# Kernel tuning notes

Measured on AMD Instinct MI355X. Metric: run time of the kernel, lower is better.

The kernel has to match this reference:

```python
import jax, jax.numpy as jnp
import numpy as np

N_NODES = 50000
N_EDGES = 800000
HID = 128
EDGE_IN = 2 * HID + 4 + 20  # 2*hidden + edge_feat_dim + num_r_gaussian = 280


def setup_inputs() -> dict:
    key = jax.random.key(0)
    ks = jax.random.split(key, 16)
    s = lambda fan_in: 1.0 / np.sqrt(fan_in)
    inp = {
        "h": jax.random.normal(ks[0], (N_NODES, HID), dtype=jnp.float32),
        "edge_index": jax.random.randint(ks[1], (2, N_EDGES), 0, N_NODES, dtype=jnp.int64) if jax.config.jax_enable_x64 else jax.random.randint(ks[1], (2, N_EDGES), 0, N_NODES, dtype=jnp.int32),
        "edge_attr": jax.random.normal(ks[2], (N_EDGES, 24), dtype=jnp.float32),
        # edge_mlp: Linear(280->128) relu Linear(128->128) relu (act_last=True)
        "We1": jax.random.uniform(ks[3], (EDGE_IN, HID), jnp.float32, -s(EDGE_IN), s(EDGE_IN)),
        "be1": jnp.zeros((HID,), jnp.float32),
        "We2": jax.random.uniform(ks[4], (HID, HID), jnp.float32, -s(HID), s(HID)),
        "be2": jnp.zeros((HID,), jnp.float32),
        # edge_inf: Linear(128->1) + sigmoid
        "Wg": jax.random.uniform(ks[5], (HID, 1), jnp.float32, -s(HID), s(HID)),
        "bg": jnp.zeros((1,), jnp.float32),
        # node_mlp: Linear(256->128) relu Linear(128->128)
        "Wn1": jax.random.uniform(ks[6], (2 * HID, HID), jnp.float32, -s(2 * HID), s(2 * HID)),
        "bn1": jnp.zeros((HID,), jnp.float32),
        "Wn2": jax.random.uniform(ks[7], (HID, HID), jnp.float32, -s(HID), s(HID)),
        "bn2": jnp.zeros((HID,), jnp.float32),
    }
    return inp


def reference(h, edge_index, edge_attr, We1, be1, We2, be2, Wg, bg, Wn1, bn1, Wn2, bn2):
    dst, src = edge_index[0], edge_index[1]
    hi, hj = h[dst], h[src]                       # [E, HID] each
    x = jnp.concatenate([edge_attr, hi, hj], -1)  # [E, 280]
    mij = jax.nn.relu(jax.nn.relu(x @ We1 + be1) @ We2 + be2)  # [E, HID]
    eij = jax.nn.sigmoid(mij @ Wg + bg)           # [E, 1]
    mi = jax.ops.segment_sum(mij * eij, dst, num_segments=h.shape[0])  # [N, HID]
    y = jnp.concatenate([mi, h], -1)              # [N, 2*HID]
    out = jax.nn.relu(y @ Wn1 + bn1) @ Wn2 + bn2  # [N, HID]
    return out
```

## Files before the change

kernel.cpp:

```cpp
#include <hip/hip_runtime.h>

#define N_NODES 50000
#define N_EDGES 800000
#define HID 128

typedef _Float16 f16;
typedef _Float16 half8 __attribute__((ext_vector_type(8)));
typedef _Float16 half4 __attribute__((ext_vector_type(4)));
typedef _Float16 half2v __attribute__((ext_vector_type(2)));
typedef float f32x4 __attribute__((ext_vector_type(4)));
typedef float f32x2 __attribute__((ext_vector_type(2)));

#define OFF_MI     0UL
#define OFF_H16C   25600000UL
#define OFF_WC     38400000UL
#define OFF_CNT    38604800UL
#define OFF_CUR    38805504UL
#define OFF_E4     39006208UL
#define CSR_TOTAL  51806208UL

#define OFF_FMI  0UL
#define OFF_FH16 25600000UL
#define OFF_FW   38400000UL

#define WB1 0
#define WB2 36864
#define WN1 53248
#define WN2 86016

#define TS 136
#define YS 264
#define AS 40

#define EB 32
#define NB 32

__global__ __launch_bounds__(256) void pack_weights(
    const float* __restrict__ We1, const float* __restrict__ We2,
    const float* __restrict__ Wn1, const float* __restrict__ Wn2,
    f16* __restrict__ W, int* __restrict__ cnt, float* __restrict__ mi) {
  int i = blockIdx.x * 256 + threadIdx.x;
  if (cnt && i < 50176) cnt[i] = 0;
  if (mi) {
    f32x4 z = {0.f, 0.f, 0.f, 0.f};
    for (int j = i; j < N_NODES * HID / 4; j += 102400)
      ((f32x4*)mi)[j] = z;
  }
  if (i < 36864) {
    int j = i & 7, n = (i >> 3) & 127, qk = i >> 10;
    int k = qk * 8 + j;
    float v = 0.f;
    if (k < 256) v = We1[(24 + k) * 128 + n];
    else if (k < 280) v = We1[(k - 256) * 128 + n];
    W[WB1 + i] = (f16)v;
  } else if (i < 53248) {
    int l = i - 36864;
    int j = l & 7, n = (l >> 3) & 127, qk = l >> 10;
    W[WB2 + l] = (f16)We2[(qk * 8 + j) * 128 + n];
  } else if (i < 86016) {
    int l = i - 53248;
    int j = l & 7, n = (l >> 3) & 127, qk = l >> 10;
    W[WN1 + l] = (f16)Wn1[(qk * 8 + j) * 128 + n];
  } else if (i < 102400) {
    int l = i - 86016;
    int j = l & 7, n = (l >> 3) & 127, qk = l >> 10;
    W[WN2 + l] = (f16)Wn2[(qk * 8 + j) * 128 + n];
  }
}

__global__ __launch_bounds__(256) void scan_kernel(const int* __restrict__ cnt,
                                                   int* __restrict__ cur) {
  __shared__ int red[4];
  __shared__ int wsum[4];
  int t = threadIdx.x, b = blockIdx.x;
  int lane = t & 63, w = t >> 6;
  int s0 = 0;
  for (int i = t * 4; i < b * 1024; i += 1024) {
    int4 v = *(const int4*)(cnt + i);
    s0 += v.x + v.y + v.z + v.w;
  }
  #pragma unroll
  for (int off = 32; off; off >>= 1) s0 += __shfl_down(s0, off, 64);
  if (lane == 0) red[w] = s0;
  __syncthreads();
  int base_all = red[0] + red[1] + red[2] + red[3];
  int base = b * 1024 + t * 4;
  int4 v = *(const int4*)(cnt + base);
  int s = v.x + v.y + v.z + v.w;
  int inc = s;
  #pragma unroll
  for (int off = 1; off < 64; off <<= 1) {
    int u = __shfl_up(inc, off, 64);
    if (lane >= off) inc += u;
  }
  if (lane == 63) wsum[w] = inc;
  __syncthreads();
  int wbase = 0;
  for (int i = 0; i < w; ++i) wbase += wsum[i];
  int excl = base_all + wbase + inc - s;
  int4 o;
  o.x = excl; o.y = excl + v.x; o.z = o.y + v.y; o.w = o.z + v.z;
  *(int4*)(cur + base) = o;
}

__global__ __launch_bounds__(256) void fill_perm(
    const int* __restrict__ eidx, int* __restrict__ cur, int4* __restrict__ e4) {
  int i = blockIdx.x * 256 + threadIdx.x;
  int d = eidx[i];
  int s = eidx[N_EDGES + i];
  int p = atomicAdd(&cur[d], 1);
  int4 rec; rec.x = i; rec.y = d; rec.z = s; rec.w = 0;
  e4[p] = rec;
}

__global__ __launch_bounds__(256, 8) void precompute_kernel(
    const float* __restrict__ h, const int* __restrict__ eidx,
    const f16* __restrict__ Wp, f16* __restrict__ P,
    f16* __restrict__ h16, int* __restrict__ cnt) {
  __shared__ f16 Y[NB * 136];
  int t = threadIdx.x;
  int n0 = blockIdx.x * NB;
  {
    int rb = t >> 4, ch = t & 15;
    #pragma unroll
    for (int p = 0; p < 2; ++p) {
      int r = p * 16 + rb;
      int g = n0 + r; if (g >= N_NODES) g = N_NODES - 1;
      const float4* s4 = (const float4*)(h + (size_t)g * HID + ch * 8);
      float4 a = s4[0], b = s4[1];
      half8 v = {(f16)a.x, (f16)a.y, (f16)a.z, (f16)a.w,
                 (f16)b.x, (f16)b.y, (f16)b.z, (f16)b.w};
      *(half8*)&Y[r * 136 + ch * 8] = v;
      *(half8*)(h16 + (size_t)g * HID + ch * 8) = v;
    }
  }
  if (cnt) {
    for (int i = blockIdx.x * 256 + t; i < N_EDGES; i += gridDim.x * 256)
      atomicAdd(&cnt[eidx[i]], 1);
  }
  __syncthreads();
  int w = t >> 6, lane = t & 63, q = lane >> 4, c = lane & 15;
  int colBase = w * 32;
  const f16* B = Wp + WB1 + ((size_t)(q * 128 + colBase + c)) * 8;
  f32x4 aD[2][2], aS[2][2];
  #pragma unroll
  for (int mt = 0; mt < 2; ++mt) {
    aD[mt][0] = (f32x4){0, 0, 0, 0}; aD[mt][1] = (f32x4){0, 0, 0, 0};
    aS[mt][0] = (f32x4){0, 0, 0, 0}; aS[mt][1] = (f32x4){0, 0, 0, 0};
  }
  #pragma unroll
  for (int ks = 0; ks < 4; ++ks) {
    half8 bD0 = *(const half8*)(B + ks * 4096);
    half8 bD1 = *(const half8*)(B + ks * 4096 + 128);
    half8 bS0 = *(const half8*)(B + (ks + 4) * 4096);
    half8 bS1 = *(const half8*)(B + (ks + 4) * 4096 + 128);
    #pragma unroll
    for (int mt = 0; mt < 2; ++mt) {
      half8 a = *(const half8*)&Y[(mt * 16 + c) * 136 + ks * 32 + q * 8];
      aD[mt][0] = __builtin_amdgcn_mfma_f32_16x16x32_f16(a, bD0, aD[mt][0], 0, 0, 0);
      aD[mt][1] = __builtin_amdgcn_mfma_f32_16x16x32_f16(a, bD1, aD[mt][1], 0, 0, 0);
      aS[mt][0] = __builtin_amdgcn_mfma_f32_16x16x32_f16(a, bS0, aS[mt][0], 0, 0, 0);
      aS[mt][1] = __builtin_amdgcn_mfma_f32_16x16x32_f16(a, bS1, aS[mt][1], 0, 0, 0);
    }
  }
  #pragma unroll
  for (int mt = 0; mt < 2; ++mt)
    #pragma unroll
    for (int r = 0; r < 4; ++r) {
      int g = n0 + mt * 16 + q * 4 + r;
      if (g < N_NODES) {
        f16* o = P + (size_t)g * 256 + colBase + c;
        o[0]        = (f16)aD[mt][0][r];
        o[16]       = (f16)aD[mt][1][r];
        o[128]      = (f16)aS[mt][0][r];
        o[128 + 16] = (f16)aS[mt][1][r];
      }
    }
}

__global__ __launch_bounds__(256, 8) void edge_kernel(
    const f16* __restrict__ P, const int* __restrict__ eidx,
    const float* __restrict__ eattr,
    const f16* __restrict__ Wp, const float* __restrict__ be1,
    const float* __restrict__ be2,
    const float* __restrict__ Wg, const float* __restrict__ bg,
    float* __restrict__ mi, const int4* __restrict__ e4) {
  __shared__ f16 S16[EB * TS];
  __shared__ f16 A[EB * AS];
  __shared__ float part[EB * 4];
  __shared__ float eijL[EB];
  __shared__ int dstL[EB];
  int t = threadIdx.x;
  int bid = (blockIdx.x & 7) * 3125 + (blockIdx.x >> 3);
  int e0 = bid * EB;

  if (t < EB) dstL[t] = e4 ? e4[e0 + t].y : eidx[e0 + t];

  {
    int rb = t >> 4, ch = t & 15;
    #pragma unroll
    for (int p = 0; p < 2; ++p) {
      int r = p * 16 + rb;
      int d, s;
      if (e4) {
        int4 rec = e4[e0 + r];
        d = rec.y; s = rec.z;
      } else {
        d = eidx[e0 + r]; s = eidx[N_EDGES + e0 + r];
      }
      half8 pd = *(const half8*)(P + (size_t)d * 256 + ch * 8);
      half8 ps = *(const half8*)(P + (size_t)s * 256 + 128 + ch * 8);
      *(half8*)&S16[r * TS + ch * 8] = pd + ps;
    }
  }
  if (t < 192) {
    int el = t / 6, kk = t % 6;
    int e = e4 ? e4[e0 + el].x : (e0 + el);
    float4 f = *(const float4*)(eattr + (size_t)e * 24 + kk * 4);
    half4 hv = {(f16)f.x, (f16)f.y, (f16)f.z, (f16)f.w};
    *(half4*)&A[el * AS + kk * 4] = hv;
  }
  if (t < EB) { uint4 z = {0, 0, 0, 0}; *(uint4*)&A[t * AS + 24] = z; }
  __syncthreads();

  int w = t >> 6, lane = t & 63, q = lane >> 4, c = lane & 15;
  int colBase = w * 32;

  f32x4 acc[2][2];
  {
    float b0 = be1[colBase + c], b1 = be1[colBase + 16 + c];
    #pragma unroll
    for (int mt = 0; mt < 2; ++mt) {
      acc[mt][0] = (f32x4){b0, b0, b0, b0};
      acc[mt][1] = (f32x4){b1, b1, b1, b1};
    }
  }
  {
    const f16* bA = Wp + WB1 + 32768 + ((size_t)(q * 128 + colBase + c)) * 8;
    half8 b0f = *(const half8*)(bA);
    half8 b1f = *(const half8*)(bA + 128);
    #pragma unroll
    for (int mt = 0; mt < 2; ++mt) {
      half8 a = *(const half8*)&A[(mt * 16 + c) * AS + q * 8];
      acc[mt][0] = __builtin_amdgcn_mfma_f32_16x16x32_f16(a, b0f, acc[mt][0], 0, 0, 0);
      acc[mt][1] = __builtin_amdgcn_mfma_f32_16x16x32_f16(a, b1f, acc[mt][1], 0, 0, 0);
    }
  }
  #pragma unroll
  for (int mt = 0; mt < 2; ++mt)
    #pragma unroll
    for (int r = 0; r < 4; ++r) {
      const f16* sr = &S16[(mt * 16 + q * 4 + r) * TS + colBase + c];
      acc[mt][0][r] += (float)sr[0];
      acc[mt][1][r] += (float)sr[16];
    }

  const f16* bp2base = Wp + WB2 + ((size_t)(q * 128 + colBase + c)) * 8;
  half8 d0 = *(const half8*)(bp2base);
  half8 d1 = *(const half8*)(bp2base + 128);

  __syncthreads();
  f16* T = S16;
  #pragma unroll
  for (int mt = 0; mt < 2; ++mt)
    #pragma unroll
    for (int nt = 0; nt < 2; ++nt)
      #pragma unroll
      for (int r = 0; r < 4; ++r) {
        float v = acc[mt][nt][r];
        T[(mt * 16 + q * 4 + r) * TS + colBase + nt * 16 + c] = (f16)(v > 0.f ? v : 0.f);
      }
  __syncthreads();

  f32x4 m2[2][2];
  {
    float b0 = be2[colBase + c], b1 = be2[colBase + 16 + c];
    #pragma unroll
    for (int mt = 0; mt < 2; ++mt) {
      m2[mt][0] = (f32x4){b0, b0, b0, b0};
      m2[mt][1] = (f32x4){b1, b1, b1, b1};
    }
  }
  #pragma unroll
  for (int kk = 0; kk < 4; ++kk) {
    half8 n0, n1;
    if (kk < 3) {
      n0 = *(const half8*)(bp2base + (kk + 1) * 4096);
      n1 = *(const half8*)(bp2base + (kk + 1) * 4096 + 128);
    }
    #pragma unroll
    for (int mt = 0; mt < 2; ++mt) {
      half8 a = *(const half8*)&T[(mt * 16 + c) * TS + kk * 32 + q * 8];
      m2[mt][0] = __builtin_amdgcn_mfma_f32_16x16x32_f16(a, d0, m2[mt][0], 0, 0, 0);
      m2[mt][1] = __builtin_amdgcn_mfma_f32_16x16x32_f16(a, d1, m2[mt][1], 0, 0, 0);
    }
    d0 = n0; d1 = n1;
  }

  float wg0 = Wg[colBase + c], wg1 = Wg[colBase + 16 + c];
  float pd[2][4];
  #pragma unroll
  for (int mt = 0; mt < 2; ++mt)
    #pragma unroll
    for (int r = 0; r < 4; ++r) {
      float v0 = m2[mt][0][r]; v0 = v0 > 0.f ? v0 : 0.f; m2[mt][0][r] = v0;
      float v1 = m2[mt][1][r]; v1 = v1 > 0.f ? v1 : 0.f; m2[mt][1][r] = v1;
      pd[mt][r] = v0 * wg0 + v1 * wg1;
    }
  #pragma unroll
  for (int off = 1; off < 16; off <<= 1)
    #pragma unroll
    for (int mt = 0; mt < 2; ++mt)
      #pragma unroll
      for (int r = 0; r < 4; ++r)
        pd[mt][r] += __shfl_xor(pd[mt][r], off, 64);
  if (c == 0)
    #pragma unroll
    for (int mt = 0; mt < 2; ++mt)
      #pragma unroll
      for (int r = 0; r < 4; ++r)
        part[(mt * 16 + q * 4 + r) * 4 + w] = pd[mt][r];
  __syncthreads();
  if (t < EB) {
    float s = part[t * 4] + part[t * 4 + 1] + part[t * 4 + 2] + part[t * 4 + 3] + bg[0];
    eijL[t] = 1.f / (1.f + __expf(-s));
  }
  __syncthreads();

  if (e4) {
    #pragma unroll
    for (int mt = 0; mt < 2; ++mt)
      #pragma unroll
      for (int r = 0; r < 4; ++r) {
        int el = mt * 16 + q * 4 + r;
        float ev = eijL[el];
        T[el * TS + colBase + c]      = (f16)(m2[mt][0][r] * ev);
        T[el * TS + colBase + 16 + c] = (f16)(m2[mt][1][r] * ev);
      }
    __syncthreads();
    int cp = t & 63, grp = t >> 6;
    int r0 = grp * 8;
    float ax = 0.f, ay = 0.f;
    int dprev = dstL[r0];
    #pragma unroll
    for (int r2 = 0; r2 < 8; ++r2) {
      int rr = r0 + r2;
      half2v v = *(const half2v*)&T[rr * TS + 2 * cp];
      ax += (float)v[0]; ay += (float)v[1];
      int dnext = (r2 == 7) ? -1 : dstL[rr + 1];
      if (dnext != dprev) {
        float* base = &mi[(size_t)dprev * HID + 2 * cp];
        atomicAdd(base, ax); atomicAdd(base + 1, ay);
        ax = 0.f; ay = 0.f; dprev = dnext;
      }
    }
  } else {
    #pragma unroll
    for (int mt = 0; mt < 2; ++mt)
      #pragma unroll
      for (int r = 0; r < 4; ++r) {
        int el = mt * 16 + q * 4 + r;
        float ev = eijL[el];
        float* base = mi + (size_t)dstL[el] * HID + colBase + c;
        atomicAdd(base,      m2[mt][0][r] * ev);
        atomicAdd(base + 16, m2[mt][1][r] * ev);
      }
  }
}

__global__ __launch_bounds__(256, 8) void node_kernel(
    const float* __restrict__ mi, const f16* __restrict__ h16,
    const f16* __restrict__ Wp, const float* __restrict__ bn1,
    const float* __restrict__ bn2, float* __restrict__ out) {
  __shared__ f16 Y[NB * YS];
  int t = threadIdx.x;
  int n0 = blockIdx.x * NB;
  {
    int rb = t >> 4, ch = t & 15;
    #pragma unroll
    for (int p = 0; p < 2; ++p) {
      int r = p * 16 + rb;
      int g = n0 + r; if (g >= N_NODES) g = N_NODES - 1;
      const float4* s = (const float4*)(mi + (size_t)g * HID + ch * 8);
      float4 a = s[0], b = s[1];
      half8 v = {(f16)a.x, (f16)a.y, (f16)a.z, (f16)a.w,
                 (f16)b.x, (f16)b.y, (f16)b.z, (f16)b.w};
      *(half8*)&Y[r * YS + ch * 8] = v;
      *(uint4*)&Y[r * YS + 128 + ch * 8] = *(const uint4*)(h16 + (size_t)g * HID + ch * 8);
    }
  }
  __syncthreads();
  int w = t >> 6, lane = t & 63, q = lane >> 4, c = lane & 15;
  int colBase = w * 32;
  const f16* BN1 = Wp + WN1;
  const f16* BN2 = Wp + WN2;
  f32x4 acc[2][2];
  {
    float b0 = bn1[colBase + c], b1 = bn1[colBase + 16 + c];
    #pragma unroll
    for (int mt = 0; mt < 2; ++mt) {
      acc[mt][0] = (f32x4){b0, b0, b0, b0};
      acc[mt][1] = (f32x4){b1, b1, b1, b1};
    }
  }
  const f16* bn1base = BN1 + ((size_t)(q * 128 + colBase + c)) * 8;
  half8 bf0 = *(const half8*)(bn1base);
  half8 bf1 = *(const half8*)(bn1base + 128);
  #pragma unroll
  for (int ks = 0; ks < 8; ++ks) {
    half8 nb0, nb1;
    if (ks < 7) {
      nb0 = *(const half8*)(bn1base + (ks + 1) * 4096);
      nb1 = *(const half8*)(bn1base + (ks + 1) * 4096 + 128);
    }
    #pragma unroll
    for (int mt = 0; mt < 2; ++mt) {
      half8 a = *(const half8*)&Y[(mt * 16 + c) * YS + ks * 32 + q * 8];
      acc[mt][0] = __builtin_amdgcn_mfma_f32_16x16x32_f16(a, bf0, acc[mt][0], 0, 0, 0);
      acc[mt][1] = __builtin_amdgcn_mfma_f32_16x16x32_f16(a, bf1, acc[mt][1], 0, 0, 0);
    }
    bf0 = nb0; bf1 = nb1;
  }
  const f16* bn2base = BN2 + ((size_t)(q * 128 + colBase + c)) * 8;
  half8 d0 = *(const half8*)(bn2base);
  half8 d1 = *(const half8*)(bn2base + 128);
  __syncthreads();
  f16* T = Y;
  #pragma unroll
  for (int mt = 0; mt < 2; ++mt)
    #pragma unroll
    for (int nt = 0; nt < 2; ++nt)
      #pragma unroll
      for (int r = 0; r < 4; ++r) {
        float v = acc[mt][nt][r];
        T[(mt * 16 + q * 4 + r) * TS + colBase + nt * 16 + c] = (f16)(v > 0.f ? v : 0.f);
      }
  __syncthreads();
  f32x4 m2[2][2];
  {
    float b0 = bn2[colBase + c], b1 = bn2[colBase + 16 + c];
    #pragma unroll
    for (int mt = 0; mt < 2; ++mt) {
      m2[mt][0] = (f32x4){b0, b0, b0, b0};
      m2[mt][1] = (f32x4){b1, b1, b1, b1};
    }
  }
  #pragma unroll
  for (int kk = 0; kk < 4; ++kk) {
    half8 n0, n1;
    if (kk < 3) {
      n0 = *(const half8*)(bn2base + (kk + 1) * 4096);
      n1 = *(const half8*)(bn2base + (kk + 1) * 4096 + 128);
    }
    #pragma unroll
    for (int mt = 0; mt < 2; ++mt) {
      half8 a = *(const half8*)&T[(mt * 16 + c) * TS + kk * 32 + q * 8];
      m2[mt][0] = __builtin_amdgcn_mfma_f32_16x16x32_f16(a, d0, m2[mt][0], 0, 0, 0);
      m2[mt][1] = __builtin_amdgcn_mfma_f32_16x16x32_f16(a, d1, m2[mt][1], 0, 0, 0);
    }
    d0 = n0; d1 = n1;
  }
  #pragma unroll
  for (int mt = 0; mt < 2; ++mt)
    #pragma unroll
    for (int r = 0; r < 4; ++r) {
      int g = n0 + mt * 16 + q * 4 + r;
      if (g < N_NODES) {
        float* o = out + (size_t)g * HID + colBase + c;
        o[0]  = m2[mt][0][r];
        o[16] = m2[mt][1][r];
      }
    }
}

extern "C" void kernel_launch(void* const* d_in, const int* in_sizes, int n_in,
                              void* d_out, int out_size, void* d_ws, size_t ws_size,
                              hipStream_t stream) {
  const float* h    = (const float*)d_in[0];
  const int*   eidx = (const int*)d_in[1];
  const float* eattr= (const float*)d_in[2];
  const float* We1  = (const float*)d_in[3];
  const float* be1  = (const float*)d_in[4];
  const float* We2  = (const float*)d_in[5];
  const float* be2  = (const float*)d_in[6];
  const float* Wg   = (const float*)d_in[7];
  const float* bg   = (const float*)d_in[8];
  const float* Wn1  = (const float*)d_in[9];
  const float* bn1  = (const float*)d_in[10];
  const float* Wn2  = (const float*)d_in[11];
  const float* bn2  = (const float*)d_in[12];
  float* out = (float*)d_out;
  char* ws = (char*)d_ws;

  if (ws_size >= CSR_TOTAL) {
    float* mi  = (float*)(ws + OFF_MI);
    f16* h16   = (f16*)(ws + OFF_H16C);
    f16* Wp    = (f16*)(ws + OFF_WC);
    int* cnt   = (int*)(ws + OFF_CNT);
    int* cur   = (int*)(ws + OFF_CUR);
    int4* e4   = (int4*)(ws + OFF_E4);
    f16* P     = (f16*)out;

    pack_weights<<<400, 256, 0, stream>>>(We1, We2, Wn1, Wn2, Wp, cnt, mi);
    precompute_kernel<<<(N_NODES + NB - 1) / NB, 256, 0, stream>>>(h, eidx, Wp, P, h16, cnt);
    scan_kernel<<<49, 256, 0, stream>>>(cnt, cur);
    fill_perm<<<3125, 256, 0, stream>>>(eidx, cur, e4);
    edge_kernel<<<N_EDGES / EB, 256, 0, stream>>>(P, eidx, eattr, Wp, be1, be2,
                                                  Wg, bg, mi, e4);
    node_kernel<<<(N_NODES + NB - 1) / NB, 256, 0, stream>>>(mi, h16, Wp, bn1, bn2, out);
  } else {
    float* mi  = (float*)(ws + OFF_FMI);
    f16*   h16 = (f16*)(ws + OFF_FH16);
    f16*   Wp  = (f16*)(ws + OFF_FW);
    f16*   P   = (f16*)out;

    pack_weights<<<400, 256, 0, stream>>>(We1, We2, Wn1, Wn2, Wp, nullptr, mi);
    precompute_kernel<<<(N_NODES + NB - 1) / NB, 256, 0, stream>>>(h, eidx, Wp, P, h16, nullptr);
    edge_kernel<<<N_EDGES / EB, 256, 0, stream>>>(P, eidx, eattr, Wp, be1, be2,
                                                  Wg, bg, mi, nullptr);
    node_kernel<<<(N_NODES + NB - 1) / NB, 256, 0, stream>>>(mi, h16, Wp, bn1, bn2, out);
  }
}
```

Baseline: 425.5 us.

## Stage precompute outputs through LDS for coalesced stores; widen segmented atomic runs

The precompute kernel now writes its MFMA results into a widened shared tile and then stores P rows with coalesced 16-byte vector writes, replacing scattered 2-byte global stores. In the CSR edge path, each thread now reduces one column over 16 sorted edges instead of two columns over 8, so runs of equal destination are longer and fewer atomics are issued. The cost is extra shared memory, two more barriers in precompute, and scalar LDS reads in the edge reduction.

```diff
diff --git a/kernel.cpp b/kernel.cpp
--- a/kernel.cpp
+++ b/kernel.cpp
@@ -30,6 +30,7 @@
 
 #define TS 136
 #define YS 264
+#define PS 264
 #define AS 40
 
 #define EB 32
@@ -117,7 +118,7 @@
     const float* __restrict__ h, const int* __restrict__ eidx,
     const f16* __restrict__ Wp, f16* __restrict__ P,
     f16* __restrict__ h16, int* __restrict__ cnt) {
-  __shared__ f16 Y[NB * 136];
+  __shared__ f16 Y[NB * PS];
   int t = threadIdx.x;
   int n0 = blockIdx.x * NB;
   {
@@ -130,7 +131,7 @@
       float4 a = s4[0], b = s4[1];
       half8 v = {(f16)a.x, (f16)a.y, (f16)a.z, (f16)a.w,
                  (f16)b.x, (f16)b.y, (f16)b.z, (f16)b.w};
-      *(half8*)&Y[r * 136 + ch * 8] = v;
+      *(half8*)&Y[r * PS + ch * 8] = v;
       *(half8*)(h16 + (size_t)g * HID + ch * 8) = v;
     }
   }
@@ -156,26 +157,35 @@
     half8 bS1 = *(const half8*)(B + (ks + 4) * 4096 + 128);
     #pragma unroll
     for (int mt = 0; mt < 2; ++mt) {
-      half8 a = *(const half8*)&Y[(mt * 16 + c) * 136 + ks * 32 + q * 8];
+      half8 a = *(const half8*)&Y[(mt * 16 + c) * PS + ks * 32 + q * 8];
       aD[mt][0] = __builtin_amdgcn_mfma_f32_16x16x32_f16(a, bD0, aD[mt][0], 0, 0, 0);
       aD[mt][1] = __builtin_amdgcn_mfma_f32_16x16x32_f16(a, bD1, aD[mt][1], 0, 0, 0);
       aS[mt][0] = __builtin_amdgcn_mfma_f32_16x16x32_f16(a, bS0, aS[mt][0], 0, 0, 0);
       aS[mt][1] = __builtin_amdgcn_mfma_f32_16x16x32_f16(a, bS1, aS[mt][1], 0, 0, 0);
     }
   }
+  __syncthreads();
   #pragma unroll
   for (int mt = 0; mt < 2; ++mt)
     #pragma unroll
     for (int r = 0; r < 4; ++r) {
-      int g = n0 + mt * 16 + q * 4 + r;
-      if (g < N_NODES) {
-        f16* o = P + (size_t)g * 256 + colBase + c;
-        o[0]        = (f16)aD[mt][0][r];
-        o[16]       = (f16)aD[mt][1][r];
-        o[128]      = (f16)aS[mt][0][r];
-        o[128 + 16] = (f16)aS[mt][1][r];
-      }
-    }
+      int row = mt * 16 + q * 4 + r;
+      f16* o = &Y[row * PS + colBase];
+      o[c]            = (f16)aD[mt][0][r];
+      o[c + 16]       = (f16)aD[mt][1][r];
+      o[c + 128]      = (f16)aS[mt][0][r];
+      o[c + 128 + 16] = (f16)aS[mt][1][r];
+    }
+  __syncthreads();
+  #pragma unroll
+  for (int i = 0; i < 4; ++i) {
+    int idx = i * 256 + t;
+    int row = idx >> 5;
+    int off = (idx & 31) * 8;
+    int g = n0 + row;
+    if (g < N_NODES)
+      *(half8*)(P + (size_t)g * 256 + off) = *(const half8*)&Y[row * PS + off];
+  }
 }
 
 __global__ __launch_bounds__(256, 8) void edge_kernel(
@@ -338,20 +348,19 @@
         T[el * TS + colBase + 16 + c] = (f16)(m2[mt][1][r] * ev);
       }
     __syncthreads();
-    int cp = t & 63, grp = t >> 6;
-    int r0 = grp * 8;
-    float ax = 0.f, ay = 0.f;
+    int col = t & 127, half = t >> 7;
+    int r0 = half * 16;
+    float acc2 = 0.f;
     int dprev = dstL[r0];
     #pragma unroll
-    for (int r2 = 0; r2 < 8; ++r2) {
+    for (int r2 = 0; r2 < 16; ++r2) {
       int rr = r0 + r2;
-      half2v v = *(const half2v*)&T[rr * TS + 2 * cp];
-      ax += (float)v[0]; ay += (float)v[1];
-      int dnext = (r2 == 7) ? -1 : dstL[rr + 1];
+      acc2 += (float)T[rr * TS + col];
+      int dnext = (r2 == 15) ? -1 : dstL[rr + 1];
       if (dnext != dprev) {
-        float* base = &mi[(size_t)dprev * HID + 2 * cp];
-        atomicAdd(base, ax); atomicAdd(base + 1, ay);
-        ax = 0.f; ay = 0.f; dprev = dnext;
+        atomicAdd(&mi[(size_t)dprev * HID + col], acc2);
+        acc2 = 0.f;
+        dprev = dnext;
       }
     }
   } else {
```

Result: faster. 399.9 us (-6.0%).

## Pack fp16 edge attributes into sorted 64B edge records during permutation fill

Applied to the files above, without the earlier changes.

fill_perm now converts each edge's 24 float attributes to fp16 and writes them, together with dst and src, into a 64-byte record at the sorted position. The edge kernel then reads the attributes contiguously from the sorted records instead of gathering fp32 rows through the original edge id, which removes a scattered read. The segmented reduction before the atomics is also changed so each thread sums 16 rows of one column instead of 8 rows of two columns. This can cut the number of atomics when destinations repeat, but it needs a much larger workspace, so the fast path only runs if the workspace holds about 90MB.

```diff
diff --git a/kernel.cpp b/kernel.cpp
--- a/kernel.cpp
+++ b/kernel.cpp
@@ -11,13 +11,16 @@
 typedef float f32x4 __attribute__((ext_vector_type(4)));
 typedef float f32x2 __attribute__((ext_vector_type(2)));
 
+struct __align__(64) ERec { int dst, src, p0, p1; f16 attr[24]; };
+static_assert(sizeof(ERec) == 64, "ERec must be 64B");
+
 #define OFF_MI     0UL
 #define OFF_H16C   25600000UL
 #define OFF_WC     38400000UL
 #define OFF_CNT    38604800UL
 #define OFF_CUR    38805504UL
 #define OFF_E4     39006208UL
-#define CSR_TOTAL  51806208UL
+#define CSR_TOTAL  90206208UL
 
 #define OFF_FMI  0UL
 #define OFF_FH16 25600000UL
@@ -104,13 +107,26 @@
 }
 
 __global__ __launch_bounds__(256) void fill_perm(
-    const int* __restrict__ eidx, int* __restrict__ cur, int4* __restrict__ e4) {
+    const int* __restrict__ eidx, const float* __restrict__ eattr,
+    int* __restrict__ cur, ERec* __restrict__ e4) {
   int i = blockIdx.x * 256 + threadIdx.x;
   int d = eidx[i];
   int s = eidx[N_EDGES + i];
+  const float4* af = (const float4*)(eattr + (size_t)i * 24);
+  float4 f0 = af[0], f1 = af[1], f2 = af[2], f3 = af[3], f4 = af[4], f5 = af[5];
+  half8 ha = {(f16)f0.x, (f16)f0.y, (f16)f0.z, (f16)f0.w,
+              (f16)f1.x, (f16)f1.y, (f16)f1.z, (f16)f1.w};
+  half8 hb = {(f16)f2.x, (f16)f2.y, (f16)f2.z, (f16)f2.w,
+              (f16)f3.x, (f16)f3.y, (f16)f3.z, (f16)f3.w};
+  half8 hc = {(f16)f4.x, (f16)f4.y, (f16)f4.z, (f16)f4.w,
+              (f16)f5.x, (f16)f5.y, (f16)f5.z, (f16)f5.w};
   int p = atomicAdd(&cur[d], 1);
-  int4 rec; rec.x = i; rec.y = d; rec.z = s; rec.w = 0;
-  e4[p] = rec;
+  ERec* o = e4 + p;
+  int4 hd; hd.x = d; hd.y = s; hd.z = 0; hd.w = 0;
+  *(int4*)o = hd;
+  *(half8*)(o->attr)      = ha;
+  *(half8*)(o->attr + 8)  = hb;
+  *(half8*)(o->attr + 16) = hc;
 }
 
 __global__ __launch_bounds__(256, 8) void precompute_kernel(
@@ -184,7 +200,7 @@
     const f16* __restrict__ Wp, const float* __restrict__ be1,
     const float* __restrict__ be2,
     const float* __restrict__ Wg, const float* __restrict__ bg,
-    float* __restrict__ mi, const int4* __restrict__ e4) {
+    float* __restrict__ mi, const ERec* __restrict__ e4) {
   __shared__ f16 S16[EB * TS];
   __shared__ f16 A[EB * AS];
   __shared__ float part[EB * 4];
@@ -194,7 +210,7 @@
   int bid = (blockIdx.x & 7) * 3125 + (blockIdx.x >> 3);
   int e0 = bid * EB;
 
-  if (t < EB) dstL[t] = e4 ? e4[e0 + t].y : eidx[e0 + t];
+  if (t < EB) dstL[t] = e4 ? e4[e0 + t].dst : eidx[e0 + t];
 
   {
     int rb = t >> 4, ch = t & 15;
@@ -203,8 +219,8 @@
       int r = p * 16 + rb;
       int d, s;
       if (e4) {
-        int4 rec = e4[e0 + r];
-        d = rec.y; s = rec.z;
+        int2 hd = *(const int2*)(e4 + e0 + r);
+        d = hd.x; s = hd.y;
       } else {
         d = eidx[e0 + r]; s = eidx[N_EDGES + e0 + r];
       }
@@ -213,12 +229,18 @@
       *(half8*)&S16[r * TS + ch * 8] = pd + ps;
     }
   }
-  if (t < 192) {
-    int el = t / 6, kk = t % 6;
-    int e = e4 ? e4[e0 + el].x : (e0 + el);
-    float4 f = *(const float4*)(eattr + (size_t)e * 24 + kk * 4);
-    half4 hv = {(f16)f.x, (f16)f.y, (f16)f.z, (f16)f.w};
-    *(half4*)&A[el * AS + kk * 4] = hv;
+  if (e4) {
+    if (t < 96) {
+      int row = t / 3, seg = t - row * 3;
+      *(half8*)&A[row * AS + seg * 8] = *(const half8*)(e4[e0 + row].attr + seg * 8);
+    }
+  } else {
+    if (t < 192) {
+      int el = t / 6, kk = t % 6;
+      float4 f = *(const float4*)(eattr + (size_t)(e0 + el) * 24 + kk * 4);
+      half4 hv = {(f16)f.x, (f16)f.y, (f16)f.z, (f16)f.w};
+      *(half4*)&A[el * AS + kk * 4] = hv;
+    }
   }
   if (t < EB) { uint4 z = {0, 0, 0, 0}; *(uint4*)&A[t * AS + 24] = z; }
   __syncthreads();
@@ -338,20 +360,19 @@
         T[el * TS + colBase + 16 + c] = (f16)(m2[mt][1][r] * ev);
       }
     __syncthreads();
-    int cp = t & 63, grp = t >> 6;
-    int r0 = grp * 8;
-    float ax = 0.f, ay = 0.f;
+    int col = t & 127, half = t >> 7;
+    int r0 = half * 16;
+    float acc2 = 0.f;
     int dprev = dstL[r0];
     #pragma unroll
-    for (int r2 = 0; r2 < 8; ++r2) {
+    for (int r2 = 0; r2 < 16; ++r2) {
       int rr = r0 + r2;
-      half2v v = *(const half2v*)&T[rr * TS + 2 * cp];
-      ax += (float)v[0]; ay += (float)v[1];
-      int dnext = (r2 == 7) ? -1 : dstL[rr + 1];
+      acc2 += (float)T[rr * TS + col];
+      int dnext = (r2 == 15) ? -1 : dstL[rr + 1];
       if (dnext != dprev) {
-        float* base = &mi[(size_t)dprev * HID + 2 * cp];
-        atomicAdd(base, ax); atomicAdd(base + 1, ay);
-        ax = 0.f; ay = 0.f; dprev = dnext;
+        atomicAdd(&mi[(size_t)dprev * HID + col], acc2);
+        acc2 = 0.f;
+        dprev = dnext;
       }
     }
   } else {
@@ -498,13 +519,13 @@
     f16* Wp    = (f16*)(ws + OFF_WC);
     int* cnt   = (int*)(ws + OFF_CNT);
     int* cur   = (int*)(ws + OFF_CUR);
-    int4* e4   = (int4*)(ws + OFF_E4);
+    ERec* e4   = (ERec*)(ws + OFF_E4);
     f16* P     = (f16*)out;
 
     pack_weights<<<400, 256, 0, stream>>>(We1, We2, Wn1, Wn2, Wp, cnt, mi);
     precompute_kernel<<<(N_NODES + NB - 1) / NB, 256, 0, stream>>>(h, eidx, Wp, P, h16, cnt);
     scan_kernel<<<49, 256, 0, stream>>>(cnt, cur);
-    fill_perm<<<3125, 256, 0, stream>>>(eidx, cur, e4);
+    fill_perm<<<3125, 256, 0, stream>>>(eidx, eattr, cur, e4);
     edge_kernel<<<N_EDGES / EB, 256, 0, stream>>>(P, eidx, eattr, Wp, be1, be2,
                                                   Wg, bg, mi, e4);
     node_kernel<<<(N_NODES + NB - 1) / NB, 256, 0, stream>>>(mi, h16, Wp, bn1, bn2, out);
```

New measurement: 377.9 us. -11.2%, faster.
